# Kernel tuning notes

Measured on AMD Instinct MI355X. Metric: run time of the kernel, lower is better.

Reference implementation:

```python
import jax, jax.numpy as jnp
import numpy as np

D_MODEL = 512; FPQ = 15; SEQ = 2048; BSZ = 2
D_STATE = 16; D_CONV = 4; HEADDIM = 64; NHEADS = 16
D_INNER = 1024; CONV_DIM = D_INNER + 2 * D_STATE
D_IN_PROJ = 2 * D_INNER + 2 * D_STATE + NHEADS  # 2096
D_FF = 2048  # mlp_ratio 4.0 * 512
EPS_GATE = 0.01


def _rmsnorm(x, w, eps):
    xf = x.astype(jnp.float32)
    v = jnp.mean(xf * xf, axis=-1, keepdims=True)
    return w * (xf * jax.lax.rsqrt(v + eps)).astype(x.dtype)


def _mamba2(x, inproj, convw, convb, dtbias, Alog, Dp, normw, outproj):
    b, l, _ = x.shape
    zxbcdt = x @ inproj.T                      # [b,l,2096]
    z = zxbcdt[..., :D_INNER]
    xBC = zxbcdt[..., D_INNER:D_INNER + CONV_DIM]
    dt = zxbcdt[..., D_INNER + CONV_DIM:]      # [b,l,h]
    # causal depthwise conv1d (kernel D_CONV) + SiLU
    xp = jnp.pad(xBC, ((0, 0), (D_CONV - 1, 0), (0, 0)))
    conv = convb + sum(xp[:, k:k + l, :] * convw[:, k] for k in range(D_CONV))
    xBC = jax.nn.silu(conv)
    xs = xBC[..., :D_INNER]
    Bm = xBC[..., D_INNER:D_INNER + D_STATE]   # [b,l,n]
    Cm = xBC[..., D_INNER + D_STATE:]          # [b,l,n]
    dt = jax.nn.softplus(dt + dtbias)          # [b,l,h]
    A = -jnp.exp(Alog)                         # [h]
    xh = xs.reshape(b, l, NHEADS, HEADDIM)     # [b,l,h,p]
    dA = jnp.exp(dt * A)                       # [b,l,h]

    def step(hst, inp):
        dA_t, dt_t, B_t, x_t, C_t = inp        # [b,h],[b,h],[b,n],[b,h,p],[b,n]
        hst = dA_t[:, :, None, None] * hst + jnp.einsum('bh,bn,bhp->bhpn', dt_t, B_t, x_t)
        return hst, jnp.einsum('bhpn,bn->bhp', hst, C_t)

    h0 = jnp.zeros((b, NHEADS, HEADDIM, D_STATE), x.dtype)
    _, ys = jax.lax.scan(step, h0, (dA.transpose(1, 0, 2), dt.transpose(1, 0, 2),
                                    Bm.transpose(1, 0, 2), xh.transpose(1, 0, 2, 3),
                                    Cm.transpose(1, 0, 2)))
    y = ys.transpose(1, 0, 2, 3) + Dp[None, None, :, None] * xh  # [b,l,h,p]
    y = y.reshape(b, l, D_INNER) * jax.nn.silu(z)                # gated
    y = _rmsnorm(y, normw, 1e-5)
    return y @ outproj.T


def _forward(hidden_states, norm1_w, wfc_w, wfc_b, gfc_w, gfc_b,
             f_inproj, f_convw, f_convb, f_dtbias, f_Alog, f_D, f_normw, f_outproj,
             b_inproj, b_convw, b_convb, b_dtbias, b_Alog, b_D, b_normw, b_outproj,
             norm2_w, fc1_w, fc1_b, fc2_w, fc2_b):
    residual = hidden_states
    h = _rmsnorm(hidden_states, norm1_w, 1e-6)
    bsz, seq_len, d = h.shape
    cq = FPQ + 1
    nck = seq_len // cq
    h4 = h.reshape(bsz, nck, cq, d)
    frames = h4[:, :, :FPQ, :]                       # [b,nc,FPQ,d]
    queries = h4[:, :, FPQ, :]                       # [b,nc,d]
    alpha = jax.nn.softmax(queries @ wfc_w.T + wfc_b, axis=-1)   # [b,nc,FPQ]
    agg = jnp.einsum('bcfd,bcf->bcd', frames, alpha)
    gate = jax.nn.sigmoid(queries @ gfc_w.T + gfc_b)             # [b,nc,1]
    gate = gate * (1 - 2 * EPS_GATE) + EPS_GATE
    qn = queries * (1 - gate) + agg * gate
    h4 = jnp.concatenate([frames, qn[:, :, None, :]], axis=2)
    h = h4.reshape(bsz, seq_len, d)
    out_fwd = _mamba2(h, f_inproj, f_convw, f_convb, f_dtbias, f_Alog, f_D, f_normw, f_outproj)
    out_bwd = jnp.flip(_mamba2(jnp.flip(h, 1), b_inproj, b_convw, b_convb, b_dtbias, b_Alog, b_D, b_normw, b_outproj), 1)
    h = out_fwd + out_bwd + residual
    rm = h
    h = _rmsnorm(h, norm2_w, 1e-6)
    h = jax.nn.silu(h @ fc1_w.T + fc1_b) @ fc2_w.T + fc2_b
    h = h + rm
    return h + residual


def setup_inputs() -> dict:
    key = jax.random.key(0)
    ks = jax.random.split(key, 16)

    def n(k, shape, s=0.02):
        return s * jax.random.normal(k, shape, jnp.float32)

    def mixer(kb):
        k = jax.random.split(kb, 6)
        dtv = jnp.exp(jax.random.uniform(k[3], (NHEADS,), minval=jnp.log(1e-3), maxval=jnp.log(0.1)))
        return dict(
            inproj=n(k[0], (D_IN_PROJ, D_MODEL)),
            convw=n(k[1], (CONV_DIM, D_CONV), 0.2),
            convb=jnp.zeros((CONV_DIM,), jnp.float32),
            dtbias=jnp.log(jnp.expm1(dtv)),
            Alog=jnp.log(jax.random.uniform(k[4], (NHEADS,), minval=1.0, maxval=16.0)),
            D=jnp.ones((NHEADS,), jnp.float32),
            normw=jnp.ones((D_INNER,), jnp.float32),
            outproj=n(k[2], (D_MODEL, D_INNER)),
        )

    mf = mixer(ks[1]); mb = mixer(ks[2])
    inp = {
        'hidden_states': jax.random.normal(ks[0], (BSZ, SEQ, D_MODEL), jnp.float32),
        'norm1_w': jnp.ones((D_MODEL,), jnp.float32),
        'wfc_w': n(ks[3], (FPQ, D_MODEL)) * 0.001,
        'wfc_b': jnp.zeros((FPQ,), jnp.float32),
        'gfc_w': n(ks[4], (1, D_MODEL)) * 0.001,
        'gfc_b': jnp.zeros((1,), jnp.float32),
        'norm2_w': jnp.ones((D_MODEL,), jnp.float32),
        'fc1_w': n(ks[5], (D_FF, D_MODEL)),
        'fc1_b': jnp.zeros((D_FF,), jnp.float32),
        'fc2_w': n(ks[6], (D_MODEL, D_FF)),
        'fc2_b': jnp.zeros((D_MODEL,), jnp.float32),
    }
    for pre, m in (('f_', mf), ('b_', mb)):
        for kname, v in m.items():
            inp[pre + kname] = v
    return inp


def reference(hidden_states, norm1_w, wfc_w, wfc_b, gfc_w, gfc_b,
              f_inproj, f_convw, f_convb, f_dtbias, f_Alog, f_D, f_normw, f_outproj,
              b_inproj, b_convw, b_convb, b_dtbias, b_Alog, b_D, b_normw, b_outproj,
              norm2_w, fc1_w, fc1_b, fc2_w, fc2_b):
    return _forward(hidden_states, norm1_w, wfc_w, wfc_b, gfc_w, gfc_b,
                    f_inproj, f_convw, f_convb, f_dtbias, f_Alog, f_D, f_normw, f_outproj,
                    b_inproj, b_convw, b_convb, b_dtbias, b_Alog, b_D, b_normw, b_outproj,
                    norm2_w, fc1_w, fc1_b, fc2_w, fc2_b)
```

## Files before the change

### kernel.cpp

```cpp
#include <hip/hip_runtime.h>
#include <math.h>

#define SEQ 2048
#define BSZ 2
#define DM 512
#define DIN 1024
#define DSTATE 16
#define NH 16
#define HD 64
#define CONVDIM 1056
#define DINPROJ 2096
#define DFF 2048
#define ROWS (BSZ*SEQ)
#define NCH 32
#define CT  (SEQ/NCH)
#define ZXW 2176
#define ZXBN 8912896ull
#define XSN 4194304ull
#define BCN 65536ull
#define DTN 65536ull
#define YN  4194304ull
#define HSN 1048576ull

typedef short bf16x8 __attribute__((ext_vector_type(8)));
typedef float f32x4  __attribute__((ext_vector_type(4)));
typedef unsigned short u16x8 __attribute__((ext_vector_type(8)));

__device__ __forceinline__ float sigf(float x){ return 1.f/(1.f+expf(-x)); }

__device__ __forceinline__ unsigned short f2bf(float f){
  union { float f; unsigned u; } v; v.f = f;
  unsigned r = (v.u + 0x7FFFu + ((v.u >> 16) & 1u)) >> 16;
  return (unsigned short)r;
}
__device__ __forceinline__ float bf2f(unsigned short h){
  union { unsigned u; float f; } v; v.u = ((unsigned)h) << 16;
  return v.f;
}

template<int N> __device__ __forceinline__ void s_wait_vmcnt(){
  if constexpr (N == 0)      asm volatile("s_waitcnt vmcnt(0)" ::: "memory");
  else if constexpr (N == 1) asm volatile("s_waitcnt vmcnt(1)" ::: "memory");
  else if constexpr (N == 2) asm volatile("s_waitcnt vmcnt(2)" ::: "memory");
  else if constexpr (N == 3) asm volatile("s_waitcnt vmcnt(3)" ::: "memory");
  else if constexpr (N == 4) asm volatile("s_waitcnt vmcnt(4)" ::: "memory");
  else                       asm volatile("s_waitcnt vmcnt(8)" ::: "memory");
}

__device__ __forceinline__ float wave_reduce(float v){
#pragma unroll
  for (int o = 32; o > 0; o >>= 1) v += __shfl_down(v, o);
  return v;
}

__device__ __forceinline__ float block_reduce_256(float v, float* sbuf){
  v = wave_reduce(v);
  int lane = threadIdx.x & 63, wid = threadIdx.x >> 6;
  if (lane == 0) sbuf[wid] = v;
  __syncthreads();
  float s = sbuf[0] + sbuf[1] + sbuf[2] + sbuf[3];
  __syncthreads();
  return s;
}

__global__ __launch_bounds__(256)
void castpad2_k(const float* __restrict__ in0, const float* __restrict__ in1,
                unsigned short* __restrict__ out0, unsigned short* __restrict__ out1,
                int N, int K, int Npad){
  int tot = Npad*K;
  int idx = blockIdx.x*256 + threadIdx.x;
  const float* in = in0; unsigned short* out = out0;
  if (idx >= tot){ idx -= tot; in = in1; out = out1; }
  if (idx >= tot) return;
  int n = idx / K, k = idx - n*K;
  out[idx] = (n < N) ? f2bf(in[(size_t)n*K + k]) : (unsigned short)0;
}

struct Cast6 {
  const float* src[6];
  unsigned short* dst[6];
  int n[6];
};
__global__ __launch_bounds__(256)
void cast6_k(Cast6 cp){
  int seg = blockIdx.y;
  int n4 = cp.n[seg] >> 2;
  int i = blockIdx.x*256 + threadIdx.x;
  if (i >= n4) return;
  const float* src = cp.src[seg];
  unsigned short* dst = cp.dst[seg];
  float4 v = *(const float4*)&src[i*4];
  ushort4 o;
  o.x = f2bf(v.x); o.y = f2bf(v.y); o.z = f2bf(v.z); o.w = f2bf(v.w);
  *(ushort4*)&dst[i*4] = o;
}

__global__ __launch_bounds__(256)
void rmsnorm512_k(const float* __restrict__ x, const float* __restrict__ w,
                  float* __restrict__ y, unsigned short* __restrict__ yb, float eps){
  __shared__ float sbuf[4];
  int r = blockIdx.x;
  const float* xr = x + (size_t)r*DM;
  float v0 = xr[threadIdx.x];
  float v1 = xr[threadIdx.x + 256];
  float ss = block_reduce_256(v0*v0 + v1*v1, sbuf);
  float rs = rsqrtf(ss*(1.f/DM) + eps);
  float o0 = w[threadIdx.x]*v0*rs;
  float o1 = w[threadIdx.x+256]*v1*rs;
  y[(size_t)r*DM + threadIdx.x]       = o0;
  y[(size_t)r*DM + threadIdx.x + 256] = o1;
  yb[(size_t)r*DM + threadIdx.x]       = f2bf(o0);
  yb[(size_t)r*DM + threadIdx.x + 256] = f2bf(o1);
}

__global__ __launch_bounds__(256)
void gated_fusion_k(float* __restrict__ h, unsigned short* __restrict__ hb,
                    const float* __restrict__ wfc_w, const float* __restrict__ wfc_b,
                    const float* __restrict__ gfc_w, const float* __restrict__ gfc_b){
  int c = blockIdx.x;
  float* base = h + (size_t)c*16*DM;
  float* qrow = base + 15*DM;
  unsigned short* qrow_b = hb + (size_t)c*16*DM + 15*DM;
  __shared__ float q[DM];
  __shared__ float dots[16];
  for (int i = threadIdx.x; i < DM; i += 256) q[i] = qrow[i];
  __syncthreads();
  int wid = threadIdx.x >> 6, lane = threadIdx.x & 63;
  for (int f = wid; f < 16; f += 4){
    const float* wf = (f < 15) ? (wfc_w + (size_t)f*DM) : gfc_w;
    float s = 0.f;
    for (int i = lane; i < DM; i += 64) s += q[i]*wf[i];
    s = wave_reduce(s);
    if (lane == 0) dots[f] = s;
  }
  __syncthreads();
  if (threadIdx.x == 0){
    float mx = -1e30f;
    for (int f = 0; f < 15; f++){ dots[f] += wfc_b[f]; mx = fmaxf(mx, dots[f]); }
    float sum = 0.f;
    for (int f = 0; f < 15; f++){ float e = expf(dots[f]-mx); dots[f] = e; sum += e; }
    float inv = 1.f/sum;
    for (int f = 0; f < 15; f++) dots[f] *= inv;
    float g = sigf(dots[15] + gfc_b[0]);
    dots[15] = g*0.98f + 0.01f;
  }
  __syncthreads();
  float gate = dots[15];
  for (int d = threadIdx.x; d < DM; d += 256){
    float agg = 0.f;
#pragma unroll
    for (int f = 0; f < 15; f++) agg += base[(size_t)f*DM + d]*dots[f];
    float qn = q[d]*(1.f-gate) + agg*gate;
    qrow[d] = qn;
    qrow_b[d] = f2bf(qn);
  }
}

template<int NW, int WM, int WN, int FM, int FN, int DEPTH, int NBUF>
__global__ __launch_bounds__(NW*64)
void mgemm_k(const unsigned short* __restrict__ A, size_t Astride,
             const unsigned short* __restrict__ W0, const unsigned short* __restrict__ W1,
             const float* __restrict__ bias, const float* __restrict__ add1,
             const float* __restrict__ add2, float* __restrict__ Cf,
             unsigned short* __restrict__ Cb, size_t Cstride,
             int K, int Nreal, int flipArg, int act){
  constexpr int BM = WM*FM*16;
  constexpr int BN = WN*FN*16;
  constexpr int NG = (BM+BN)/16;
  constexpr int L  = NG/NW;
  static_assert(NG % NW == 0, "staging must be uniform per wave");
  constexpr int BUFS = (BM+BN)*32;
  __shared__ __align__(16) unsigned short S[NBUF*BUFS];
  int tid = threadIdx.x;
  int w = tid >> 6, lane = tid & 63;
  int gx = gridDim.x;
  int nwg = gx*gridDim.y;
  int bid = blockIdx.x + gx*blockIdx.y;
  int swz = (bid & 7)*(nwg >> 3) + (bid >> 3);
  int n0 = (swz % gx)*BN, m0 = (swz / gx)*BM;
  int dir = blockIdx.z;
  const unsigned short* Aa = A + (size_t)dir*Astride;
  const unsigned short* Wd = dir ? W1 : W0;
  int flip = (flipArg < 0) ? dir : flipArg;
  int wr = w / WN, wc = w % WN;

  f32x4 acc[FM][FN];
#pragma unroll
  for (int i = 0; i < FM; i++)
#pragma unroll
    for (int j = 0; j < FN; j++)
#pragma unroll
      for (int r = 0; r < 4; r++) acc[i][j][r] = 0.f;

  const unsigned short* gp[L];
  int gdst[L];
#pragma unroll
  for (int gi = 0; gi < L; gi++){
    int g = w + gi*NW;
    int r16 = lane >> 2, cch = lane & 3;
    int r = g*16 + r16;
    const unsigned short* src;
    if (r < BM){
      int gm = m0 + r;
      if (flip) gm = (gm & ~(SEQ-1)) | ((SEQ-1) - (gm & (SEQ-1)));
      src = Aa + (size_t)gm*K;
    } else {
      src = Wd + (size_t)(n0 + (r - BM))*K;
    }
    int c2 = (cch + ((r16 >> 1) & 3)) & 3;
    gp[gi] = src + c2*8;
    gdst[gi] = g*16*32;
  }
  int aoff[FM], boff[FN];
#pragma unroll
  for (int i = 0; i < FM; i++){
    int R = wr*FM*16 + i*16 + (lane & 15);
    int slot = ((lane >> 4) - ((R >> 1) & 3)) & 3;
    aoff[i] = R*32 + slot*8;
  }
#pragma unroll
  for (int j = 0; j < FN; j++){
    int R = BM + wc*FN*16 + j*16 + (lane & 15);
    int slot = ((lane >> 4) - ((R >> 1) & 3)) & 3;
    boff[j] = R*32 + slot*8;
  }

  int T = K >> 5;
#pragma unroll
  for (int jt = 0; jt < DEPTH; jt++){
#pragma unroll
    for (int gi = 0; gi < L; gi++)
      __builtin_amdgcn_global_load_lds(
        (const __attribute__((address_space(1))) void*)(gp[gi] + (jt << 5)),
        (__attribute__((address_space(3))) void*)&S[jt*BUFS + gdst[gi]], 16, 0, 0);
  }

  int cs = 0;
  for (int t = 0; t < T; t++){
    int rem = T - 1 - t;
    if (rem >= DEPTH-1)             s_wait_vmcnt<L*(DEPTH-1)>();
    else if constexpr (DEPTH >= 3){ if (rem == 1) s_wait_vmcnt<L>(); else s_wait_vmcnt<0>(); }
    else                            s_wait_vmcnt<0>();
    __builtin_amdgcn_s_barrier();
    __builtin_amdgcn_sched_barrier(0);
    const unsigned short* buf = &S[cs*BUFS];
    bf16x8 af[FM], bfr[FN];
#pragma unroll
    for (int i = 0; i < FM; i++) af[i] = *(const bf16x8*)&buf[aoff[i]];
#pragma unroll
    for (int j = 0; j < FN; j++) bfr[j] = *(const bf16x8*)&buf[boff[j]];
    if constexpr (NBUF == DEPTH){
      asm volatile("s_waitcnt lgkmcnt(0)" ::: "memory");
      __builtin_amdgcn_sched_barrier(0);
      __builtin_amdgcn_s_barrier();
    }
    if (t + DEPTH < T){
      int ss = cs + DEPTH; if (ss >= NBUF) ss -= NBUF;
#pragma unroll
      for (int gi = 0; gi < L; gi++)
        __builtin_amdgcn_global_load_lds(
          (const __attribute__((address_space(1))) void*)(gp[gi] + ((t + DEPTH) << 5)),
          (__attribute__((address_space(3))) void*)&S[ss*BUFS + gdst[gi]], 16, 0, 0);
    }
#pragma unroll
    for (int i = 0; i < FM; i++)
#pragma unroll
      for (int j = 0; j < FN; j++)
        acc[i][j] = __builtin_amdgcn_mfma_f32_16x16x32_bf16(af[i], bfr[j], acc[i][j], 0, 0, 0);
    cs = (cs + 1 == NBUF) ? 0 : cs + 1;
  }

  float* Cfd = Cf ? Cf + (size_t)dir*Cstride : nullptr;
  unsigned short* Cbd = Cb ? Cb + (size_t)dir*Cstride : nullptr;

  if (Cbd){
    __syncthreads();
#pragma unroll
    for (int i = 0; i < FM; i++){
#pragma unroll
      for (int j = 0; j < FN; j++){
        int col = wc*FN*16 + j*16 + (lane & 15);
        float bv = bias ? bias[n0 + col] : 0.f;
#pragma unroll
        for (int r = 0; r < 4; r++){
          int row = wr*FM*16 + i*16 + (lane >> 4)*4 + r;
          float x = acc[i][j][r] + bv;
          if (act) x = x*sigf(x);
          S[row*BN + (col ^ ((row & 3) << 3))] = f2bf(x);
        }
      }
    }
    __syncthreads();
    constexpr int TOT8 = BM*BN/8;
    for (int s = tid; s < TOT8; s += NW*64){
      int idx = s*8;
      int row = idx / BN, col = idx % BN;
      u16x8 v = *(const u16x8*)&S[row*BN + (col ^ ((row & 3) << 3))];
      *(u16x8*)&Cbd[(size_t)(m0 + row)*Nreal + n0 + col] = v;
    }
    return;
  }

  int mbase = m0 + wr*FM*16 + (lane >> 4)*4;
  int nbase = n0 + wc*FN*16 + (lane & 15);
#pragma unroll
  for (int i = 0; i < FM; i++){
#pragma unroll
    for (int j = 0; j < FN; j++){
      int col = nbase + j*16;
      if (col < Nreal){
        float bv = bias ? bias[col] : 0.f;
#pragma unroll
        for (int r = 0; r < 4; r++){
          size_t idx = (size_t)(mbase + i*16 + r)*Nreal + col;
          float x = acc[i][j][r] + bv;
          if (act) x = x*sigf(x);
          if (add1) x += add1[idx] + add2[idx];
          Cfd[idx] = x;
        }
      }
    }
  }
}

__global__ __launch_bounds__(256)
void conv_dt_k(const unsigned short* __restrict__ zxb,
               const float* __restrict__ convw0, const float* __restrict__ convw1,
               const float* __restrict__ convb0, const float* __restrict__ convb1,
               const float* __restrict__ dtbias0, const float* __restrict__ dtbias1,
               const float* __restrict__ Alog0, const float* __restrict__ Alog1,
               unsigned short* __restrict__ xs, float* __restrict__ Bm, float* __restrict__ Cm,
               float* __restrict__ dtv, float* __restrict__ dAv){
  int dir = blockIdx.z;
  const unsigned short* zb = zxb + (size_t)dir*ZXBN;
  const float* convw = dir ? convw1 : convw0;
  const float* convb = dir ? convb1 : convb0;
  int r0 = blockIdx.y*4;
  int l0 = r0 & (SEQ-1);
  int rbase = r0 - l0;
  int c = blockIdx.x*256 + threadIdx.x;
  if (c < CONVDIM){
    float w0 = convw[c*4+0], w1 = convw[c*4+1], w2 = convw[c*4+2], w3 = convw[c*4+3];
    float bv = convb[c];
    float v[7];
#pragma unroll
    for (int i = 0; i < 7; i++){
      int ls = l0 - 3 + i;
      v[i] = (ls >= 0) ? bf2f(zb[(size_t)(rbase+ls)*ZXW + 1024 + c]) : 0.f;
    }
#pragma unroll
    for (int j = 0; j < 4; j++){
      float acc = bv + v[j]*w0 + v[j+1]*w1 + v[j+2]*w2 + v[j+3]*w3;
      float val = acc*sigf(acc);
      int r = r0 + j;
      if (c < DIN) xs[(size_t)dir*XSN + (size_t)r*DIN + c] = f2bf(val);
      else if (c < DIN + DSTATE) Bm[(size_t)dir*BCN + (size_t)r*DSTATE + (c - DIN)] = val;
      else Cm[(size_t)dir*BCN + (size_t)r*DSTATE + (c - DIN - DSTATE)] = val;
    }
  } else if (blockIdx.x == 4 && threadIdx.x >= 64 && threadIdx.x < 128){
    const float* dtbias = dir ? dtbias1 : dtbias0;
    const float* Alog   = dir ? Alog1 : Alog0;
    int i = threadIdx.x - 64;
    int j = i >> 4, hh = i & 15;
    int r = r0 + j;
    float x = bf2f(zb[(size_t)r*ZXW + 2080 + hh]) + dtbias[hh];
    float sp = (x > 20.f) ? x : log1pf(expf(x));
    dtv[(size_t)dir*DTN + (size_t)r*NH + hh] = sp;
    dAv[(size_t)dir*DTN + (size_t)r*NH + hh] = expf(-expf(Alog[hh])*sp);
  }
}

__global__ __launch_bounds__(64)
void scanA_k(const unsigned short* __restrict__ xs, const float* __restrict__ Bm,
             const float* __restrict__ Cm, const float* __restrict__ dtv,
             const float* __restrict__ dAv, unsigned short* __restrict__ y,
             float* __restrict__ Hs, float* __restrict__ Ps){
  int gb = blockIdx.x;
  int dir = gb >> 10;
  int idx = gb & 1023;
  int c = idx & (NCH-1);
  int h = (idx >> 5) & 15;
  int b = idx >> 9;
  int p = threadIdx.x;
  int t0 = c*CT;
  __shared__ __align__(16) float sB[CT][16];
  __shared__ __align__(16) float sC[CT][16];
  __shared__ float sdt[CT];
  __shared__ float sdA[CT];
  const unsigned short* xb = xs + (size_t)dir*XSN + ((size_t)b*SEQ + t0)*DIN + h*HD;
  unsigned short* yb = y + (size_t)dir*YN + ((size_t)b*SEQ + t0)*DIN + h*HD;
  const float* Bb  = Bm + (size_t)dir*BCN + ((size_t)b*SEQ + t0)*DSTATE;
  const float* Cb  = Cm + (size_t)dir*BCN + ((size_t)b*SEQ + t0)*DSTATE;
  const float* dtb = dtv + (size_t)dir*DTN + ((size_t)b*SEQ + t0)*NH + h;
  const float* dAb = dAv + (size_t)dir*DTN + ((size_t)b*SEQ + t0)*NH + h;
#pragma unroll
  for (int k = 0; k < (CT*16)/64; k++){
    int i = p + k*64;
    ((float*)sB)[i] = Bb[i];
    ((float*)sC)[i] = Cb[i];
  }
  if (p < CT){
    sdt[p] = dtb[(size_t)p*NH];
    sdA[p] = dAb[(size_t)p*NH];
  }
  __syncthreads();

  float hst[16];
#pragma unroll
  for (int n = 0; n < 16; n++) hst[n] = 0.f;
  float P = 1.f;
  float xcur[16], xnxt[16];
#pragma unroll
  for (int j = 0; j < 16; j++) xcur[j] = bf2f(xb[(size_t)j*DIN + p]);

  for (int tt = 0; tt < CT; tt += 16){
    bool pf = (tt + 16 < CT);
    if (pf){
#pragma unroll
      for (int j = 0; j < 16; j++) xnxt[j] = bf2f(xb[(size_t)(tt+16+j)*DIN + p]);
    }
#pragma unroll
    for (int j = 0; j < 16; j++){
      int t = tt + j;
      float xv = xcur[j]*sdt[t];
      float dA = sdA[t];
      P *= dA;
      float4 b0 = *(const float4*)&sB[t][0];
      float4 b1 = *(const float4*)&sB[t][4];
      float4 b2 = *(const float4*)&sB[t][8];
      float4 b3 = *(const float4*)&sB[t][12];
      hst[0]  = fmaf(dA, hst[0],  b0.x*xv);
      hst[1]  = fmaf(dA, hst[1],  b0.y*xv);
      hst[2]  = fmaf(dA, hst[2],  b0.z*xv);
      hst[3]  = fmaf(dA, hst[3],  b0.w*xv);
      hst[4]  = fmaf(dA, hst[4],  b1.x*xv);
      hst[5]  = fmaf(dA, hst[5],  b1.y*xv);
      hst[6]  = fmaf(dA, hst[6],  b1.z*xv);
      hst[7]  = fmaf(dA, hst[7],  b1.w*xv);
      hst[8]  = fmaf(dA, hst[8],  b2.x*xv);
      hst[9]  = fmaf(dA, hst[9],  b2.y*xv);
      hst[10] = fmaf(dA, hst[10], b2.z*xv);
      hst[11] = fmaf(dA, hst[11], b2.w*xv);
      hst[12] = fmaf(dA, hst[12], b3.x*xv);
      hst[13] = fmaf(dA, hst[13], b3.y*xv);
      hst[14] = fmaf(dA, hst[14], b3.z*xv);
      hst[15] = fmaf(dA, hst[15], b3.w*xv);
      float4 c0 = *(const float4*)&sC[t][0];
      float4 c1 = *(const float4*)&sC[t][4];
      float4 c2 = *(const float4*)&sC[t][8];
      float4 c3 = *(const float4*)&sC[t][12];
      float a0 = hst[0]*c0.x;  a0 = fmaf(hst[1],  c0.y, a0);
      a0 = fmaf(hst[2],  c0.z, a0); a0 = fmaf(hst[3],  c0.w, a0);
      float a1 = hst[4]*c1.x;  a1 = fmaf(hst[5],  c1.y, a1);
      a1 = fmaf(hst[6],  c1.z, a1); a1 = fmaf(hst[7],  c1.w, a1);
      float a2 = hst[8]*c2.x;  a2 = fmaf(hst[9],  c2.y, a2);
      a2 = fmaf(hst[10], c2.z, a2); a2 = fmaf(hst[11], c2.w, a2);
      float a3 = hst[12]*c3.x; a3 = fmaf(hst[13], c3.y, a3);
      a3 = fmaf(hst[14], c3.z, a3); a3 = fmaf(hst[15], c3.w, a3);
      yb[(size_t)t*DIN + p] = f2bf((a0+a1)+(a2+a3));
    }
    if (pf){
#pragma unroll
      for (int j = 0; j < 16; j++) xcur[j] = xnxt[j];
    }
  }
  size_t base = (size_t)dir*HSN + ((size_t)((b*NH + h)*NCH + c))*1024;
#pragma unroll
  for (int n = 0; n < 16; n++) Hs[base + n*64 + p] = hst[n];
  if (p == 0) Ps[dir*1024 + (b*NH + h)*NCH + c] = P;
}

__global__ __launch_bounds__(64)
void scanC_k(const float* __restrict__ Cm, const float* __restrict__ dAv,
             const float* __restrict__ Hs, const float* __restrict__ Ps,
             unsigned short* __restrict__ y){
  int gb = blockIdx.x;
  int dir = gb >> 10;
  int idx = gb & 1023;
  int c = idx & (NCH-1);
  if (c == 0) return;
  int h = (idx >> 5) & 15;
  int b = idx >> 9;
  int p = threadIdx.x;
  int t0 = c*CT;
  int bh = b*NH + h;
  float hstart[16];
#pragma unroll
  for (int n = 0; n < 16; n++) hstart[n] = 0.f;
  for (int j = 0; j < c; j++){
    float Pj = Ps[dir*1024 + bh*NCH + j];
    const float* Hj = Hs + (size_t)dir*HSN + ((size_t)(bh*NCH + j))*1024;
#pragma unroll
    for (int n = 0; n < 16; n++) hstart[n] = fmaf(Pj, hstart[n], Hj[n*64 + p]);
  }
  __shared__ __align__(16) float sC[CT][16];
  __shared__ float sdA[CT];
  const float* Cb  = Cm + (size_t)dir*BCN + ((size_t)b*SEQ + t0)*DSTATE;
  const float* dAb = dAv + (size_t)dir*DTN + ((size_t)b*SEQ + t0)*NH + h;
  unsigned short* yb = y + (size_t)dir*YN + ((size_t)b*SEQ + t0)*DIN + h*HD;
#pragma unroll
  for (int k = 0; k < (CT*16)/64; k++){
    int i = p + k*64;
    ((float*)sC)[i] = Cb[i];
  }
  if (p < CT) sdA[p] = dAb[(size_t)p*NH];
  __syncthreads();

  float cp = 1.f;
  float ycur[16], ynxt[16];
#pragma unroll
  for (int j = 0; j < 16; j++) ycur[j] = bf2f(yb[(size_t)j*DIN + p]);
  for (int tt = 0; tt < CT; tt += 16){
    bool pf = (tt + 16 < CT);
    if (pf){
#pragma unroll
      for (int j = 0; j < 16; j++) ynxt[j] = bf2f(yb[(size_t)(tt+16+j)*DIN + p]);
    }
#pragma unroll
    for (int j = 0; j < 16; j++){
      int t = tt + j;
      cp *= sdA[t];
      float4 c0 = *(const float4*)&sC[t][0];
      float4 c1 = *(const float4*)&sC[t][4];
      float4 c2 = *(const float4*)&sC[t][8];
      float4 c3 = *(const float4*)&sC[t][12];
      float a0 = hstart[0]*c0.x;  a0 = fmaf(hstart[1],  c0.y, a0);
      a0 = fmaf(hstart[2],  c0.z, a0); a0 = fmaf(hstart[3],  c0.w, a0);
      float a1 = hstart[4]*c1.x;  a1 = fmaf(hstart[5],  c1.y, a1);
      a1 = fmaf(hstart[6],  c1.z, a1); a1 = fmaf(hstart[7],  c1.w, a1);
      float a2 = hstart[8]*c2.x;  a2 = fmaf(hstart[9],  c2.y, a2);
      a2 = fmaf(hstart[10], c2.z, a2); a2 = fmaf(hstart[11], c2.w, a2);
      float a3 = hstart[12]*c3.x; a3 = fmaf(hstart[13], c3.y, a3);
      a3 = fmaf(hstart[14], c3.z, a3); a3 = fmaf(hstart[15], c3.w, a3);
      float dot = (a0+a1)+(a2+a3);
      yb[(size_t)t*DIN + p] = f2bf(ycur[j] + cp*dot);
    }
    if (pf){
#pragma unroll
      for (int j = 0; j < 16; j++) ycur[j] = ynxt[j];
    }
  }
}

__global__ __launch_bounds__(256)
void gated_rms_k(const unsigned short* __restrict__ y, const unsigned short* __restrict__ xs,
                 const unsigned short* __restrict__ zxb,
                 const float* __restrict__ Dp0, const float* __restrict__ Dp1,
                 const float* __restrict__ nw0, const float* __restrict__ nw1,
                 unsigned short* __restrict__ out){
  __shared__ float sbuf[4];
  int r = blockIdx.x;
  int dir = blockIdx.y;
  const float* Dp = dir ? Dp1 : Dp0;
  const float* normw = dir ? nw1 : nw0;
  const unsigned short* yr = y + (size_t)dir*YN + (size_t)r*DIN;
  const unsigned short* xr = xs + (size_t)dir*XSN + (size_t)r*DIN;
  const unsigned short* zr = zxb + (size_t)dir*ZXBN + (size_t)r*ZXW;
  unsigned short* outr = out + (size_t)dir*((size_t)ROWS*DIN) + (size_t)r*DIN;
  int d0 = threadIdx.x*4;
  ushort4 yu4 = *(const ushort4*)&yr[d0];
  ushort4 xu4 = *(const ushort4*)&xr[d0];
  ushort4 zu4 = *(const ushort4*)&zr[d0];
  float Dv = Dp[d0 >> 6];
  float vals[4]; float ss = 0.f;
  float yv[4] = {bf2f(yu4.x), bf2f(yu4.y), bf2f(yu4.z), bf2f(yu4.w)};
  float xv[4] = {bf2f(xu4.x), bf2f(xu4.y), bf2f(xu4.z), bf2f(xu4.w)};
  float zv[4] = {bf2f(zu4.x), bf2f(zu4.y), bf2f(zu4.z), bf2f(zu4.w)};
#pragma unroll
  for (int i = 0; i < 4; i++){
    float g = (yv[i] + Dv*xv[i]) * (zv[i]*sigf(zv[i]));
    vals[i] = g; ss += g*g;
  }
  ss = block_reduce_256(ss, sbuf);
  float rs = rsqrtf(ss*(1.f/DIN) + 1e-5f);
  ushort4 o;
  o.x = f2bf(normw[d0+0]*vals[0]*rs);
  o.y = f2bf(normw[d0+1]*vals[1]*rs);
  o.z = f2bf(normw[d0+2]*vals[2]*rs);
  o.w = f2bf(normw[d0+3]*vals[3]*rs);
  *(ushort4*)&outr[d0] = o;
}

__global__ __launch_bounds__(256)
void addres_rms_k(const float* __restrict__ outf, const float* __restrict__ outb,
                  const float* __restrict__ hid, const float* __restrict__ w,
                  float* __restrict__ hsum, unsigned short* __restrict__ h2b){
  __shared__ float sbuf[4];
  int r = blockIdx.x;
  int l = r & (SEQ-1);
  int rb = (r - l) + ((SEQ-1) - l);
  float vals[2]; float ss = 0.f;
#pragma unroll
  for (int i = 0; i < 2; i++){
    int d = threadIdx.x + i*256;
    float v = outf[(size_t)r*DM + d] + outb[(size_t)rb*DM + d] + hid[(size_t)r*DM + d];
    hsum[(size_t)r*DM + d] = v;
    vals[i] = v; ss += v*v;
  }
  ss = block_reduce_256(ss, sbuf);
  float rs = rsqrtf(ss*(1.f/DM) + 1e-6f);
#pragma unroll
  for (int i = 0; i < 2; i++){
    int d = threadIdx.x + i*256;
    h2b[(size_t)r*DM + d] = f2bf(w[d]*vals[i]*rs);
  }
}

extern "C" void kernel_launch(void* const* d_in, const int* in_sizes, int n_in,
                              void* d_out, int out_size, void* d_ws, size_t ws_size,
                              hipStream_t stream){
  const float* hid     = (const float*)d_in[0];
  const float* norm1_w = (const float*)d_in[1];
  const float* wfc_w   = (const float*)d_in[2];
  const float* wfc_b   = (const float*)d_in[3];
  const float* gfc_w   = (const float*)d_in[4];
  const float* gfc_b   = (const float*)d_in[5];
  const float* norm2_w = (const float*)d_in[6];
  const float* fc1_w   = (const float*)d_in[7];
  const float* fc1_b   = (const float*)d_in[8];
  const float* fc2_w   = (const float*)d_in[9];
  const float* fc2_b   = (const float*)d_in[10];
  const float* inproj[2]  = {(const float*)d_in[11], (const float*)d_in[19]};
  const float* convw[2]   = {(const float*)d_in[12], (const float*)d_in[20]};
  const float* convb[2]   = {(const float*)d_in[13], (const float*)d_in[21]};
  const float* dtbias[2]  = {(const float*)d_in[14], (const float*)d_in[22]};
  const float* Alog[2]    = {(const float*)d_in[15], (const float*)d_in[23]};
  const float* Dp[2]      = {(const float*)d_in[16], (const float*)d_in[24]};
  const float* normw[2]   = {(const float*)d_in[17], (const float*)d_in[25]};
  const float* outproj[2] = {(const float*)d_in[18], (const float*)d_in[26]};

  float* ws = (float*)d_ws;
  unsigned short* zxb = (unsigned short*)ws;
  float* xsf   = ws + 8912896;
  unsigned short* xsb = (unsigned short*)xsf;
  float* Bmb   = xsf + 4194304;
  float* Cmb   = Bmb + 2*BCN;
  float* dtv   = Cmb + 2*BCN;
  float* dAv   = dtv + 2*DTN;
  float* ysc   = dAv + 2*DTN;
  unsigned short* ysc_b = (unsigned short*)ysc;
  float* Ps    = ysc + 4194304;
  float* outd  = Ps + 2048;
  float* hsum  = outd + 4194304;
  float* hnorm = hsum + 2097152;
  unsigned short* hnorm_bf = (unsigned short*)(hnorm + 2097152);
  unsigned short* ysc_bf   = (unsigned short*)(hnorm + 2097152 + 1048576);
  unsigned short* wbf      = (unsigned short*)(hnorm + 2097152 + 1048576 + 4194304);
  float* Hs = hsum;
  unsigned short* a1_bf = (unsigned short*)zxb;
  unsigned short* h2_bf = xsb;
  unsigned short* wi0 = wbf,            * wi1 = wbf + 1114112;
  unsigned short* wo0 = wbf + 2228224,  * wo1 = wbf + 2752512;
  unsigned short* wf1 = wbf + 3276800;
  unsigned short* wf2 = wbf + 4325376;
  size_t need_bytes = (size_t)34146304*4;
  if (ws_size < need_bytes) return;

  castpad2_k<<<(2*2176*512)/256, 256, 0, stream>>>(inproj[0], inproj[1], wi0, wi1, 2096, 512, 2176);
  Cast6 cp;
  cp.src[0] = outproj[0]; cp.dst[0] = wo0; cp.n[0] = 512*1024;
  cp.src[1] = outproj[1]; cp.dst[1] = wo1; cp.n[1] = 512*1024;
  cp.src[2] = fc1_w; cp.dst[2] = wf1; cp.n[2] = 2048*512;
  cp.src[3] = fc2_w; cp.dst[3] = wf2; cp.n[3] = 512*2048;
  cp.src[4] = fc2_w; cp.dst[4] = wf2; cp.n[4] = 0;
  cp.src[5] = fc2_w; cp.dst[5] = wf2; cp.n[5] = 0;
  cast6_k<<<dim3((2048*512/4)/256, 4), 256, 0, stream>>>(cp);

  rmsnorm512_k<<<ROWS, 256, 0, stream>>>(hid, norm1_w, hnorm, hnorm_bf, 1e-6f);
  gated_fusion_k<<<BSZ*(SEQ/16), 256, 0, stream>>>(hnorm, hnorm_bf, wfc_w, wfc_b, gfc_w, gfc_b);

  mgemm_k<8,2,4,4,2,2,2><<<dim3(2176/128, 4096/128, 2), 512, 0, stream>>>(
      hnorm_bf, 0, wi0, wi1, nullptr, nullptr, nullptr, nullptr, zxb, ZXBN,
      512, ZXW, -1, 0);
  conv_dt_k<<<dim3(5, ROWS/4, 2), 256, 0, stream>>>(
      zxb, convw[0], convw[1], convb[0], convb[1], dtbias[0], dtbias[1],
      Alog[0], Alog[1], xsb, Bmb, Cmb, dtv, dAv);
  scanA_k<<<2*BSZ*NH*NCH, 64, 0, stream>>>(xsb, Bmb, Cmb, dtv, dAv, ysc_b, Hs, Ps);
  scanC_k<<<2*BSZ*NH*NCH, 64, 0, stream>>>(Cmb, dAv, Hs, Ps, ysc_b);
  gated_rms_k<<<dim3(ROWS, 2), 256, 0, stream>>>(
      ysc_b, xsb, zxb, Dp[0], Dp[1], normw[0], normw[1], ysc_bf);
  mgemm_k<8,2,4,2,1,3,4><<<dim3(512/64, 4096/64, 2), 512, 0, stream>>>(
      ysc_bf, (size_t)ROWS*DIN, wo0, wo1, nullptr, nullptr, nullptr,
      outd, nullptr, 2097152, 1024, DM, 0, 0);

  addres_rms_k<<<ROWS, 256, 0, stream>>>(outd, outd + 2097152, hid, norm2_w, hsum, h2_bf);
  mgemm_k<8,2,4,4,2,3,3><<<dim3(2048/128, 4096/128, 1), 512, 0, stream>>>(
      h2_bf, 0, wf1, wf1, fc1_b, nullptr, nullptr, nullptr, a1_bf, 0,
      512, DFF, 0, 1);
  mgemm_k<8,2,4,2,1,3,4><<<dim3(512/64, 4096/64, 1), 512, 0, stream>>>(
      a1_bf, 0, wf2, wf2, fc2_b, hsum, hid, (float*)d_out, nullptr, 0,
      2048, DM, 0, 0);
}
```

Baseline: 197.9 us.

## Fuse causal conv+SiLU and D skip into chunked scan, drop xs buffer

The depthwise causal conv and SiLU for the 1024 x-channels move out of the conv kernel and into scanA. scanA now reads the raw pre-conv columns straight from the in-projection output, keeping a 3-element carry window. scanA also adds the D*x skip term, so gated_rms no longer reads xs, and the intermediate xs buffer is removed, shrinking the workspace. This cuts a full write and two full reads of a bf16 activation tensor. In exchange, the serial scan loop gets extra per-step work (a 4-tap conv and a sigmoid), which may lengthen the latency-bound recurrence.

```diff
diff --git a/kernel.cpp b/kernel.cpp
--- a/kernel.cpp
+++ b/kernel.cpp
@@ -16,7 +16,6 @@
 #define CT  (SEQ/NCH)
 #define ZXW 2176
 #define ZXBN 8912896ull
-#define XSN 4194304ull
 #define BCN 65536ull
 #define DTN 65536ull
 #define YN  4194304ull
@@ -323,44 +322,45 @@
   }
 }
 
-__global__ __launch_bounds__(256)
-void conv_dt_k(const unsigned short* __restrict__ zxb,
-               const float* __restrict__ convw0, const float* __restrict__ convw1,
-               const float* __restrict__ convb0, const float* __restrict__ convb1,
-               const float* __restrict__ dtbias0, const float* __restrict__ dtbias1,
-               const float* __restrict__ Alog0, const float* __restrict__ Alog1,
-               unsigned short* __restrict__ xs, float* __restrict__ Bm, float* __restrict__ Cm,
-               float* __restrict__ dtv, float* __restrict__ dAv){
-  int dir = blockIdx.z;
+__global__ __launch_bounds__(128)
+void convbc_dt_k(const unsigned short* __restrict__ zxb,
+                 const float* __restrict__ convw0, const float* __restrict__ convw1,
+                 const float* __restrict__ convb0, const float* __restrict__ convb1,
+                 const float* __restrict__ dtbias0, const float* __restrict__ dtbias1,
+                 const float* __restrict__ Alog0, const float* __restrict__ Alog1,
+                 float* __restrict__ Bm, float* __restrict__ Cm,
+                 float* __restrict__ dtv, float* __restrict__ dAv){
+  int dir = blockIdx.y;
   const unsigned short* zb = zxb + (size_t)dir*ZXBN;
-  const float* convw = dir ? convw1 : convw0;
-  const float* convb = dir ? convb1 : convb0;
-  int r0 = blockIdx.y*4;
+  int r0 = blockIdx.x*4;
   int l0 = r0 & (SEQ-1);
   int rbase = r0 - l0;
-  int c = blockIdx.x*256 + threadIdx.x;
-  if (c < CONVDIM){
-    float w0 = convw[c*4+0], w1 = convw[c*4+1], w2 = convw[c*4+2], w3 = convw[c*4+3];
-    float bv = convb[c];
+  int tid = threadIdx.x;
+  if (tid < 32){
+    const float* convw = dir ? convw1 : convw0;
+    const float* convb = dir ? convb1 : convb0;
+    int cc = 1024 + tid;
+    int col = 2048 + tid;
+    float w0 = convw[cc*4+0], w1 = convw[cc*4+1], w2 = convw[cc*4+2], w3 = convw[cc*4+3];
+    float bv = convb[cc];
     float v[7];
 #pragma unroll
     for (int i = 0; i < 7; i++){
       int ls = l0 - 3 + i;
-      v[i] = (ls >= 0) ? bf2f(zb[(size_t)(rbase+ls)*ZXW + 1024 + c]) : 0.f;
+      v[i] = (ls >= 0) ? bf2f(zb[(size_t)(rbase+ls)*ZXW + col]) : 0.f;
     }
 #pragma unroll
     for (int j = 0; j < 4; j++){
       float acc = bv + v[j]*w0 + v[j+1]*w1 + v[j+2]*w2 + v[j+3]*w3;
       float val = acc*sigf(acc);
       int r = r0 + j;
-      if (c < DIN) xs[(size_t)dir*XSN + (size_t)r*DIN + c] = f2bf(val);
-      else if (c < DIN + DSTATE) Bm[(size_t)dir*BCN + (size_t)r*DSTATE + (c - DIN)] = val;
-      else Cm[(size_t)dir*BCN + (size_t)r*DSTATE + (c - DIN - DSTATE)] = val;
-    }
-  } else if (blockIdx.x == 4 && threadIdx.x >= 64 && threadIdx.x < 128){
+      if (tid < 16) Bm[(size_t)dir*BCN + (size_t)r*DSTATE + tid] = val;
+      else          Cm[(size_t)dir*BCN + (size_t)r*DSTATE + (tid-16)] = val;
+    }
+  } else if (tid >= 64){
     const float* dtbias = dir ? dtbias1 : dtbias0;
     const float* Alog   = dir ? Alog1 : Alog0;
-    int i = threadIdx.x - 64;
+    int i = tid - 64;
     int j = i >> 4, hh = i & 15;
     int r = r0 + j;
     float x = bf2f(zb[(size_t)r*ZXW + 2080 + hh]) + dtbias[hh];
@@ -371,9 +371,13 @@
 }
 
 __global__ __launch_bounds__(64)
-void scanA_k(const unsigned short* __restrict__ xs, const float* __restrict__ Bm,
+void scanA_k(const unsigned short* __restrict__ zxb, const float* __restrict__ Bm,
              const float* __restrict__ Cm, const float* __restrict__ dtv,
-             const float* __restrict__ dAv, unsigned short* __restrict__ y,
+             const float* __restrict__ dAv,
+             const float* __restrict__ convw0, const float* __restrict__ convw1,
+             const float* __restrict__ convb0, const float* __restrict__ convb1,
+             const float* __restrict__ Dp0, const float* __restrict__ Dp1,
+             unsigned short* __restrict__ y,
              float* __restrict__ Hs, float* __restrict__ Ps){
   int gb = blockIdx.x;
   int dir = gb >> 10;
@@ -387,42 +391,56 @@
   __shared__ __align__(16) float sC[CT][16];
   __shared__ float sdt[CT];
   __shared__ float sdA[CT];
-  const unsigned short* xb = xs + (size_t)dir*XSN + ((size_t)b*SEQ + t0)*DIN + h*HD;
+  const unsigned short* zb = zxb + (size_t)dir*ZXBN;
+  const unsigned short* zcol = zb + ((size_t)b*SEQ)*ZXW + 1024 + h*HD + p;
   unsigned short* yb = y + (size_t)dir*YN + ((size_t)b*SEQ + t0)*DIN + h*HD;
   const float* Bb  = Bm + (size_t)dir*BCN + ((size_t)b*SEQ + t0)*DSTATE;
   const float* Cb  = Cm + (size_t)dir*BCN + ((size_t)b*SEQ + t0)*DSTATE;
   const float* dtb = dtv + (size_t)dir*DTN + ((size_t)b*SEQ + t0)*NH + h;
   const float* dAb = dAv + (size_t)dir*DTN + ((size_t)b*SEQ + t0)*NH + h;
+  const float* convw = dir ? convw1 : convw0;
+  const float* convb = dir ? convb1 : convb0;
+  float Dv = (dir ? Dp1 : Dp0)[h];
+  int ch = h*HD + p;
+  float cw0 = convw[ch*4+0], cw1 = convw[ch*4+1], cw2 = convw[ch*4+2], cw3 = convw[ch*4+3];
+  float cbv = convb[ch];
 #pragma unroll
   for (int k = 0; k < (CT*16)/64; k++){
     int i = p + k*64;
     ((float*)sB)[i] = Bb[i];
     ((float*)sC)[i] = Cb[i];
   }
-  if (p < CT){
-    sdt[p] = dtb[(size_t)p*NH];
-    sdA[p] = dAb[(size_t)p*NH];
-  }
+  sdt[p] = dtb[(size_t)p*NH];
+  sdA[p] = dAb[(size_t)p*NH];
   __syncthreads();
 
   float hst[16];
 #pragma unroll
   for (int n = 0; n < 16; n++) hst[n] = 0.f;
   float P = 1.f;
-  float xcur[16], xnxt[16];
-#pragma unroll
-  for (int j = 0; j < 16; j++) xcur[j] = bf2f(xb[(size_t)j*DIN + p]);
+  float carry0 = (t0 >= 3) ? bf2f(zcol[(size_t)(t0-3)*ZXW]) : 0.f;
+  float carry1 = (t0 >= 2) ? bf2f(zcol[(size_t)(t0-2)*ZXW]) : 0.f;
+  float carry2 = (t0 >= 1) ? bf2f(zcol[(size_t)(t0-1)*ZXW]) : 0.f;
+  float cur[16], nxt[16];
+#pragma unroll
+  for (int j = 0; j < 16; j++) cur[j] = bf2f(zcol[(size_t)(t0+j)*ZXW]);
 
   for (int tt = 0; tt < CT; tt += 16){
     bool pf = (tt + 16 < CT);
     if (pf){
 #pragma unroll
-      for (int j = 0; j < 16; j++) xnxt[j] = bf2f(xb[(size_t)(tt+16+j)*DIN + p]);
-    }
+      for (int j = 0; j < 16; j++) nxt[j] = bf2f(zcol[(size_t)(t0+tt+16+j)*ZXW]);
+    }
+    float win[19];
+    win[0] = carry0; win[1] = carry1; win[2] = carry2;
+#pragma unroll
+    for (int j = 0; j < 16; j++) win[3+j] = cur[j];
 #pragma unroll
     for (int j = 0; j < 16; j++){
       int t = tt + j;
-      float xv = xcur[j]*sdt[t];
+      float xo = cbv + win[j]*cw0 + win[j+1]*cw1 + win[j+2]*cw2 + win[j+3]*cw3;
+      float xsil = xo*sigf(xo);
+      float xv = xsil*sdt[t];
       float dA = sdA[t];
       P *= dA;
       float4 b0 = *(const float4*)&sB[t][0];
@@ -457,11 +475,13 @@
       a2 = fmaf(hst[10], c2.z, a2); a2 = fmaf(hst[11], c2.w, a2);
       float a3 = hst[12]*c3.x; a3 = fmaf(hst[13], c3.y, a3);
       a3 = fmaf(hst[14], c3.z, a3); a3 = fmaf(hst[15], c3.w, a3);
-      yb[(size_t)t*DIN + p] = f2bf((a0+a1)+(a2+a3));
-    }
+      float dot = (a0+a1)+(a2+a3);
+      yb[(size_t)t*DIN + p] = f2bf(dot + Dv*xsil);
+    }
+    carry0 = cur[13]; carry1 = cur[14]; carry2 = cur[15];
     if (pf){
 #pragma unroll
-      for (int j = 0; j < 16; j++) xcur[j] = xnxt[j];
+      for (int j = 0; j < 16; j++) cur[j] = nxt[j];
     }
   }
   size_t base = (size_t)dir*HSN + ((size_t)((b*NH + h)*NCH + c))*1024;
@@ -503,7 +523,7 @@
     int i = p + k*64;
     ((float*)sC)[i] = Cb[i];
   }
-  if (p < CT) sdA[p] = dAb[(size_t)p*NH];
+  sdA[p] = dAb[(size_t)p*NH];
   __syncthreads();
 
   float cp = 1.f;
@@ -543,32 +563,26 @@
 }
 
 __global__ __launch_bounds__(256)
-void gated_rms_k(const unsigned short* __restrict__ y, const unsigned short* __restrict__ xs,
+void gated_rms_k(const unsigned short* __restrict__ y,
                  const unsigned short* __restrict__ zxb,
-                 const float* __restrict__ Dp0, const float* __restrict__ Dp1,
                  const float* __restrict__ nw0, const float* __restrict__ nw1,
                  unsigned short* __restrict__ out){
   __shared__ float sbuf[4];
   int r = blockIdx.x;
   int dir = blockIdx.y;
-  const float* Dp = dir ? Dp1 : Dp0;
   const float* normw = dir ? nw1 : nw0;
   const unsigned short* yr = y + (size_t)dir*YN + (size_t)r*DIN;
-  const unsigned short* xr = xs + (size_t)dir*XSN + (size_t)r*DIN;
   const unsigned short* zr = zxb + (size_t)dir*ZXBN + (size_t)r*ZXW;
   unsigned short* outr = out + (size_t)dir*((size_t)ROWS*DIN) + (size_t)r*DIN;
   int d0 = threadIdx.x*4;
   ushort4 yu4 = *(const ushort4*)&yr[d0];
-  ushort4 xu4 = *(const ushort4*)&xr[d0];
   ushort4 zu4 = *(const ushort4*)&zr[d0];
-  float Dv = Dp[d0 >> 6];
   float vals[4]; float ss = 0.f;
   float yv[4] = {bf2f(yu4.x), bf2f(yu4.y), bf2f(yu4.z), bf2f(yu4.w)};
-  float xv[4] = {bf2f(xu4.x), bf2f(xu4.y), bf2f(xu4.z), bf2f(xu4.w)};
   float zv[4] = {bf2f(zu4.x), bf2f(zu4.y), bf2f(zu4.z), bf2f(zu4.w)};
 #pragma unroll
   for (int i = 0; i < 4; i++){
-    float g = (yv[i] + Dv*xv[i]) * (zv[i]*sigf(zv[i]));
+    float g = yv[i] * (zv[i]*sigf(zv[i]));
     vals[i] = g; ss += g*g;
   }
   ss = block_reduce_256(ss, sbuf);
@@ -631,9 +645,7 @@
 
   float* ws = (float*)d_ws;
   unsigned short* zxb = (unsigned short*)ws;
-  float* xsf   = ws + 8912896;
-  unsigned short* xsb = (unsigned short*)xsf;
-  float* Bmb   = xsf + 4194304;
+  float* Bmb   = ws + 8912896;
   float* Cmb   = Bmb + 2*BCN;
   float* dtv   = Cmb + 2*BCN;
   float* dAv   = dtv + 2*DTN;
@@ -648,12 +660,12 @@
   unsigned short* wbf      = (unsigned short*)(hnorm + 2097152 + 1048576 + 4194304);
   float* Hs = hsum;
   unsigned short* a1_bf = (unsigned short*)zxb;
-  unsigned short* h2_bf = xsb;
+  unsigned short* h2_bf = (unsigned short*)ysc;
   unsigned short* wi0 = wbf,            * wi1 = wbf + 1114112;
   unsigned short* wo0 = wbf + 2228224,  * wo1 = wbf + 2752512;
   unsigned short* wf1 = wbf + 3276800;
   unsigned short* wf2 = wbf + 4325376;
-  size_t need_bytes = (size_t)34146304*4;
+  size_t need_bytes = (size_t)29952000*4;
   if (ws_size < need_bytes) return;
 
   castpad2_k<<<(2*2176*512)/256, 256, 0, stream>>>(inproj[0], inproj[1], wi0, wi1, 2096, 512, 2176);
@@ -672,13 +684,15 @@
   mgemm_k<8,2,4,4,2,2,2><<<dim3(2176/128, 4096/128, 2), 512, 0, stream>>>(
       hnorm_bf, 0, wi0, wi1, nullptr, nullptr, nullptr, nullptr, zxb, ZXBN,
       512, ZXW, -1, 0);
-  conv_dt_k<<<dim3(5, ROWS/4, 2), 256, 0, stream>>>(
+  convbc_dt_k<<<dim3(ROWS/4, 2), 128, 0, stream>>>(
       zxb, convw[0], convw[1], convb[0], convb[1], dtbias[0], dtbias[1],
-      Alog[0], Alog[1], xsb, Bmb, Cmb, dtv, dAv);
-  scanA_k<<<2*BSZ*NH*NCH, 64, 0, stream>>>(xsb, Bmb, Cmb, dtv, dAv, ysc_b, Hs, Ps);
+      Alog[0], Alog[1], Bmb, Cmb, dtv, dAv);
+  scanA_k<<<2*BSZ*NH*NCH, 64, 0, stream>>>(
+      zxb, Bmb, Cmb, dtv, dAv, convw[0], convw[1], convb[0], convb[1],
+      Dp[0], Dp[1], ysc_b, Hs, Ps);
   scanC_k<<<2*BSZ*NH*NCH, 64, 0, stream>>>(Cmb, dAv, Hs, Ps, ysc_b);
   gated_rms_k<<<dim3(ROWS, 2), 256, 0, stream>>>(
-      ysc_b, xsb, zxb, Dp[0], Dp[1], normw[0], normw[1], ysc_bf);
+      ysc_b, zxb, normw[0], normw[1], ysc_bf);
   mgemm_k<8,2,4,2,1,3,4><<<dim3(512/64, 4096/64, 2), 512, 0, stream>>>(
       ysc_bf, (size_t)ROWS*DIN, wo0, wo1, nullptr, nullptr, nullptr,
       outd, nullptr, 2097152, 1024, DM, 0, 0);
```

New measurement: 195.3 us (median of 3 runs). About the same (-1.3%).

## Add inter-chunk state prefix kernel so scanC reads precomputed start states

Applied to the files above, without the earlier changes.

Adds a small scanB kernel that does the sequential prefix recurrence over chunk states once per (dir,batch,head), writing each chunk's starting state to a buffer. scanC then loads its start state directly instead of every chunk block re-accumulating all previous chunk states, which cost O(NCH^2) reads. It adds an extra kernel launch with only 64 blocks doing a serial 31-step loop, and reuses the outd buffer for the start states. The p<CT guards are also dropped, which is valid because CT equals 64.

```diff
diff --git a/kernel.cpp b/kernel.cpp
--- a/kernel.cpp
+++ b/kernel.cpp
@@ -399,10 +399,8 @@
     ((float*)sB)[i] = Bb[i];
     ((float*)sC)[i] = Cb[i];
   }
-  if (p < CT){
-    sdt[p] = dtb[(size_t)p*NH];
-    sdA[p] = dAb[(size_t)p*NH];
-  }
+  sdt[p] = dtb[(size_t)p*NH];
+  sdA[p] = dAb[(size_t)p*NH];
   __syncthreads();
 
   float hst[16];
@@ -471,8 +469,32 @@
 }
 
 __global__ __launch_bounds__(64)
+void scanB_k(const float* __restrict__ Hs, const float* __restrict__ Ps,
+             float* __restrict__ Hstart){
+  int g = blockIdx.x;
+  int dir = g >> 5;
+  int bh = g & 31;
+  int p = threadIdx.x;
+  size_t base = (size_t)dir*HSN + (size_t)bh*NCH*1024;
+  const float* Pp = Ps + dir*1024 + bh*NCH;
+  float s[16];
+#pragma unroll
+  for (int n = 0; n < 16; n++) s[n] = 0.f;
+#pragma unroll 2
+  for (int c = 1; c < NCH; c++){
+    float Pj = Pp[c-1];
+    const float* Hj = Hs + base + (size_t)(c-1)*1024;
+#pragma unroll
+    for (int n = 0; n < 16; n++) s[n] = fmaf(Pj, s[n], Hj[n*64 + p]);
+    float* Oc = Hstart + base + (size_t)c*1024;
+#pragma unroll
+    for (int n = 0; n < 16; n++) Oc[n*64 + p] = s[n];
+  }
+}
+
+__global__ __launch_bounds__(64)
 void scanC_k(const float* __restrict__ Cm, const float* __restrict__ dAv,
-             const float* __restrict__ Hs, const float* __restrict__ Ps,
+             const float* __restrict__ Hstart,
              unsigned short* __restrict__ y){
   int gb = blockIdx.x;
   int dir = gb >> 10;
@@ -485,14 +507,9 @@
   int t0 = c*CT;
   int bh = b*NH + h;
   float hstart[16];
-#pragma unroll
-  for (int n = 0; n < 16; n++) hstart[n] = 0.f;
-  for (int j = 0; j < c; j++){
-    float Pj = Ps[dir*1024 + bh*NCH + j];
-    const float* Hj = Hs + (size_t)dir*HSN + ((size_t)(bh*NCH + j))*1024;
-#pragma unroll
-    for (int n = 0; n < 16; n++) hstart[n] = fmaf(Pj, hstart[n], Hj[n*64 + p]);
-  }
+  const float* Hj = Hstart + (size_t)dir*HSN + ((size_t)(bh*NCH + c))*1024;
+#pragma unroll
+  for (int n = 0; n < 16; n++) hstart[n] = Hj[n*64 + p];
   __shared__ __align__(16) float sC[CT][16];
   __shared__ float sdA[CT];
   const float* Cb  = Cm + (size_t)dir*BCN + ((size_t)b*SEQ + t0)*DSTATE;
@@ -503,7 +520,7 @@
     int i = p + k*64;
     ((float*)sC)[i] = Cb[i];
   }
-  if (p < CT) sdA[p] = dAb[(size_t)p*NH];
+  sdA[p] = dAb[(size_t)p*NH];
   __syncthreads();
 
   float cp = 1.f;
@@ -647,6 +664,7 @@
   unsigned short* ysc_bf   = (unsigned short*)(hnorm + 2097152 + 1048576);
   unsigned short* wbf      = (unsigned short*)(hnorm + 2097152 + 1048576 + 4194304);
   float* Hs = hsum;
+  float* Hstart = outd;
   unsigned short* a1_bf = (unsigned short*)zxb;
   unsigned short* h2_bf = xsb;
   unsigned short* wi0 = wbf,            * wi1 = wbf + 1114112;
@@ -676,7 +694,8 @@
       zxb, convw[0], convw[1], convb[0], convb[1], dtbias[0], dtbias[1],
       Alog[0], Alog[1], xsb, Bmb, Cmb, dtv, dAv);
   scanA_k<<<2*BSZ*NH*NCH, 64, 0, stream>>>(xsb, Bmb, Cmb, dtv, dAv, ysc_b, Hs, Ps);
-  scanC_k<<<2*BSZ*NH*NCH, 64, 0, stream>>>(Cmb, dAv, Hs, Ps, ysc_b);
+  scanB_k<<<64, 64, 0, stream>>>(Hs, Ps, Hstart);
+  scanC_k<<<2*BSZ*NH*NCH, 64, 0, stream>>>(Cmb, dAv, Hstart, ysc_b);
   gated_rms_k<<<dim3(ROWS, 2), 256, 0, stream>>>(
       ysc_b, xsb, zxb, Dp[0], Dp[1], normw[0], normw[1], ysc_bf);
   mgemm_k<8,2,4,2,1,3,4><<<dim3(512/64, 4096/64, 2), 512, 0, stream>>>(
```

After: 202.8 us. 1.03x slower.
